# Kernel tuning notes

Measured on AMD Instinct MI355X. Metric: run time of the kernel, lower is better.

Reference implementation:

```python
import jax, jax.numpy as jnp
import numpy as np

N_INST = 2_000_000   # total instances
D_IN = 32
D_HID = 64
D_OUT = 1
NUM_BAGS = 100_000   # ids in [0, NUM_BAGS)


def setup_inputs() -> dict:
    key = jax.random.key(0)
    k0, k1, k2, k3, k4 = jax.random.split(key, 5)
    x = jax.random.normal(k0, (N_INST, D_IN), dtype=jnp.float32)
    # sorted bag ids, every bag present (contiguous bags of equal size -> a
    # valid instance of sorted_randint over [0, NUM_BAGS))
    ids = (jnp.arange(N_INST, dtype=jnp.int32) // (N_INST // NUM_BAGS))[None, :]
    W1 = jax.random.normal(k1, (D_IN, D_HID), dtype=jnp.float32) / np.sqrt(D_IN)
    b1 = jax.random.normal(k2, (D_HID,), dtype=jnp.float32) * 0.01
    W2 = jax.random.normal(k3, (D_HID, D_OUT), dtype=jnp.float32) / np.sqrt(D_HID)
    b2 = jax.random.normal(k4, (D_OUT,), dtype=jnp.float32) * 0.01
    return {"x": x, "ids": ids, "W1": W1, "b1": b1, "W2": W2, "b2": b2}


def reference(x, ids, W1, b1, W2, b2):
    inner_ids = ids[-1]                                    # [N] bag id per instance
    h = jax.nn.relu(x @ W1 + b1)                           # prepNN: [N, D_HID]
    # fused segment mean over bags (replaces the Python loop + boolean masks)
    sums = jax.ops.segment_sum(h, inner_ids, num_segments=NUM_BAGS)          # [B, D_HID]
    counts = jax.ops.segment_sum(jnp.ones((h.shape[0],), h.dtype), inner_ids,
                                 num_segments=NUM_BAGS)                      # [B]
    pooled = sums / counts[:, None]                        # aggregation_func = mean
    out = pooled @ W2 + b2                                 # afterNN: [B, D_OUT]
    return out
```

## Files before the change

kernel.cpp:

```cpp
#include <hip/hip_runtime.h>

typedef __attribute__((ext_vector_type(8))) short short8v;
typedef __attribute__((ext_vector_type(4))) int   int4v;
typedef __attribute__((ext_vector_type(4))) float f32x4;

#define NBLOCKS 1024
#define WPB 4
#define NSLOT 64

__device__ __forceinline__ unsigned short f2bf(float f) {
  unsigned u = __builtin_bit_cast(unsigned, f);
  unsigned r = u + 0x7FFFu + ((u >> 16) & 1u);
  return (unsigned short)(r >> 16);
}
__device__ __forceinline__ float bf2f(unsigned short h) {
  unsigned u = ((unsigned)h) << 16;
  return __builtin_bit_cast(float, u);
}

template <int CTRL>
__device__ __forceinline__ float dpp_add(float s) {
  int t = __builtin_amdgcn_update_dpp(0, __builtin_bit_cast(int, s), CTRL, 0xF, 0xF, true);
  return s + __builtin_bit_cast(float, t);
}

__global__ void __launch_bounds__(256) bag_mlp_v3(
    const float* __restrict__ x, const int* __restrict__ ids,
    const float* __restrict__ W1, const float* __restrict__ b1,
    const float* __restrict__ W2,
    float* __restrict__ bag_sum, int nchunks, int cpw, int nbags)
{
  __shared__ __align__(16) char stage[WPB][8192];
  __shared__ float sacc[WPB][NSLOT];

  const int wid  = threadIdx.x >> 6;
  const int lane = threadIdx.x & 63;
  const int lm = lane & 15, lg = lane >> 4;
  const int w = blockIdx.x * WPB + wid;

  const int c_begin = w * cpw;
  if (c_begin >= nchunks) return;
  const int c_end = min(c_begin + cpw, nchunks);

  sacc[wid][lane] = 0.f;
  const int base_id = ids[(size_t)c_begin * 64];

  short8v bh[4], bl[4];
#pragma unroll
  for (int nt = 0; nt < 4; ++nt) {
    const int col = lm + 16 * nt;
#pragma unroll
    for (int e = 0; e < 8; ++e) {
      const int k = 16 * (e >> 2) + 4 * lg + (e & 3);
      const float f = W1[k * 64 + col];
      const unsigned short h = f2bf(f);
      bh[nt][e] = (short)h;
      bl[nt][e] = (short)f2bf(f - bf2f(h));
    }
  }
  float b1c[4], w2c[4];
#pragma unroll
  for (int nt = 0; nt < 4; ++nt) {
    b1c[nt] = b1[lm + 16 * nt];
    w2c[nt] = W2[lm + 16 * nt];
  }

  const int R_perm = ((lm >> 2) << 4) + (lg << 2) + (lm & 3);

  auto issue_stage = [&](int c) {
    const float* src0 = x + (size_t)c * 2048;
#pragma unroll
    for (int q = 0; q < 8; ++q) {
      const int g   = q * 64 + lane;
      const int row = g >> 3;
      const int sl  = (g & 7) ^ (row & 7);
      const float* src = src0 + row * 32 + sl * 4;
      __builtin_amdgcn_global_load_lds(
          (const __attribute__((address_space(1))) void*)src,
          (__attribute__((address_space(3))) void*)(&stage[wid][q * 1024]),
          16, 0, 0);
    }
  };

  issue_stage(c_begin);

  for (int c = c_begin; c < c_end; ++c) {
    asm volatile("s_waitcnt vmcnt(0)" ::: "memory");

    const int myid = ids[(size_t)c * 64 + R_perm];

    short8v ah[4], al[4];
    const char* sb = &stage[wid][0];
#pragma unroll
    for (int t = 0; t < 4; ++t) {
      const int rb = t * 2048 + lm * 128;
      const float4 va = *(const float4*)(sb + rb + ((lg ^ (lm & 7)) << 4));
      const float4 vb = *(const float4*)(sb + rb + (((lg + 4) ^ (lm & 7)) << 4));
      int4v ahi, ali;
#pragma unroll
      for (int j = 0; j < 4; ++j) {
        const float f0 = (j < 2) ? ((j == 0) ? va.x : va.z) : ((j == 2) ? vb.x : vb.z);
        const float f1 = (j < 2) ? ((j == 0) ? va.y : va.w) : ((j == 2) ? vb.y : vb.w);
        const unsigned u0 = __builtin_bit_cast(unsigned, f0);
        const unsigned u1 = __builtin_bit_cast(unsigned, f1);
        const unsigned r0 = u0 + 0x7FFFu + ((u0 >> 16) & 1u);
        const unsigned r1 = u1 + 0x7FFFu + ((u1 >> 16) & 1u);
        const unsigned h0 = r0 & 0xFFFF0000u, h1 = r1 & 0xFFFF0000u;
        const float lo0 = f0 - __builtin_bit_cast(float, h0);
        const float lo1 = f1 - __builtin_bit_cast(float, h1);
        ahi[j] = (int)((r0 >> 16) | h1);
        ali[j] = (int)(((unsigned)f2bf(lo0)) | (((unsigned)f2bf(lo1)) << 16));
      }
      ah[t] = __builtin_bit_cast(short8v, ahi);
      al[t] = __builtin_bit_cast(short8v, ali);
    }

    asm volatile("s_waitcnt lgkmcnt(0)" ::: "memory");
    const int cnext = (c + 1 < c_end) ? c + 1 : c;
    issue_stage(cnext);

    float myval = 0.f;
#pragma unroll
    for (int t = 0; t < 4; ++t) {
      f32x4 acc[4];
#pragma unroll
      for (int nt = 0; nt < 4; ++nt)
        acc[nt] = (f32x4){b1c[nt], b1c[nt], b1c[nt], b1c[nt]};
#pragma unroll
      for (int nt = 0; nt < 4; ++nt) {
        acc[nt] = __builtin_amdgcn_mfma_f32_16x16x32_bf16(ah[t], bh[nt], acc[nt], 0, 0, 0);
        acc[nt] = __builtin_amdgcn_mfma_f32_16x16x32_bf16(ah[t], bl[nt], acc[nt], 0, 0, 0);
        acc[nt] = __builtin_amdgcn_mfma_f32_16x16x32_bf16(al[t], bh[nt], acc[nt], 0, 0, 0);
      }
      float ps[4];
#pragma unroll
      for (int r = 0; r < 4; ++r) {
        float s = 0.f;
#pragma unroll
        for (int nt = 0; nt < 4; ++nt)
          s = fmaf(fmaxf(acc[nt][r], 0.f), w2c[nt], s);
        ps[r] = s;
      }
#pragma unroll
      for (int r = 0; r < 4; ++r) {
        ps[r] = dpp_add<0xB1>(ps[r]);
        ps[r] = dpp_add<0x4E>(ps[r]);
        ps[r] = dpp_add<0x124>(ps[r]);
        ps[r] = dpp_add<0x128>(ps[r]);
      }
      const float t01 = (lm & 1) ? ps[1] : ps[0];
      const float t23 = (lm & 1) ? ps[3] : ps[2];
      const float sel = (lm & 2) ? t23 : t01;
      if ((lm >> 2) == t) myval = sel;
    }

    const int slot = myid - base_id;
    if (slot < NSLOT) atomicAdd(&sacc[wid][slot], myval);
    else              atomicAdd(&bag_sum[myid], myval);
  }

  const float v = sacc[wid][lane];
  const int bag = base_id + lane;
  if (v != 0.f && bag < nbags) atomicAdd(&bag_sum[bag], v);
}

__global__ void __launch_bounds__(256) bag_start_kernel(
    const int* __restrict__ ids, int* __restrict__ start, int n)
{
  for (int i = blockIdx.x * blockDim.x + threadIdx.x; i < n;
       i += gridDim.x * blockDim.x) {
    const int id = ids[i];
    if (i == 0 || ids[i - 1] != id) start[id] = i;
  }
}

__global__ void __launch_bounds__(256) finalize_kernel(
    const float* __restrict__ bag_sum, const int* __restrict__ start,
    const float* __restrict__ b2, float* __restrict__ out, int nbags, int n)
{
  const int b = blockIdx.x * blockDim.x + threadIdx.x;
  if (b >= nbags) return;
  const int s = start[b];
  const int e = (b + 1 < nbags) ? start[b + 1] : n;
  out[b] = bag_sum[b] / (float)(e - s) + b2[0];
}

extern "C" void kernel_launch(void* const* d_in, const int* in_sizes, int n_in,
                              void* d_out, int out_size, void* d_ws, size_t ws_size,
                              hipStream_t stream)
{
  const float* x   = (const float*)d_in[0];
  const int*   ids = (const int*)d_in[1];
  const float* W1  = (const float*)d_in[2];
  const float* b1  = (const float*)d_in[3];
  const float* W2  = (const float*)d_in[4];
  const float* b2  = (const float*)d_in[5];
  float* out = (float*)d_out;

  const int n     = in_sizes[0] / 32;
  const int nbags = out_size;

  float* bag_sum = (float*)d_ws;
  int*   start   = (int*)(bag_sum + nbags);

  (void)hipMemsetAsync(bag_sum, 0, (size_t)nbags * sizeof(float), stream);

  const int nchunks = n / 64;
  const int nwaves  = NBLOCKS * WPB;
  const int cpw     = (nchunks + nwaves - 1) / nwaves;

  bag_mlp_v3<<<NBLOCKS, 256, 0, stream>>>(x, ids, W1, b1, W2, bag_sum,
                                          nchunks, cpw, nbags);
  bag_start_kernel<<<2048, 256, 0, stream>>>(ids, start, n);
  finalize_kernel<<<(nbags + 255) / 256, 256, 0, stream>>>(bag_sum, start, b2,
                                                           out, nbags, n);
}
```

Baseline: 366.5 us.

## Prefetch next chunk into registers and use truncation for bf16 split

Replaces the direct global-to-LDS async loads with register prefetching: each iteration writes the previously loaded chunk to LDS, then issues global loads for the next chunk (and its ids) that overlap with the MFMA compute. The bf16 hi/lo split now truncates instead of rounding, which removes several integer ops per element, and launch bounds request three blocks per CU. The changes trade more register pressure and extra LDS store instructions for less exposed load latency and less conversion work. Truncation slightly changes the precision of the three-term split.

```diff
diff --git a/kernel.cpp b/kernel.cpp
--- a/kernel.cpp
+++ b/kernel.cpp
@@ -24,7 +24,7 @@
   return s + __builtin_bit_cast(float, t);
 }
 
-__global__ void __launch_bounds__(256) bag_mlp_v3(
+__global__ void __launch_bounds__(256, 3) bag_mlp_v4(
     const float* __restrict__ x, const int* __restrict__ ids,
     const float* __restrict__ W1, const float* __restrict__ b1,
     const float* __restrict__ W2,
@@ -66,58 +66,61 @@
   }
 
   const int R_perm = ((lm >> 2) << 4) + (lg << 2) + (lm & 3);
-
-  auto issue_stage = [&](int c) {
-    const float* src0 = x + (size_t)c * 2048;
-#pragma unroll
-    for (int q = 0; q < 8; ++q) {
-      const int g   = q * 64 + lane;
-      const int row = g >> 3;
-      const int sl  = (g & 7) ^ (row & 7);
-      const float* src = src0 + row * 32 + sl * 4;
-      __builtin_amdgcn_global_load_lds(
-          (const __attribute__((address_space(1))) void*)src,
-          (__attribute__((address_space(3))) void*)(&stage[wid][q * 1024]),
-          16, 0, 0);
-    }
-  };
-
-  issue_stage(c_begin);
+  const int wr_base = (lane >> 3) * 128 + ((((lane & 7) ^ ((lane >> 3) & 7))) << 4);
+  char* sb = &stage[wid][0];
+
+  float4 r0, r1, r2, r3, r4, r5, r6, r7;
+  int myid;
+  {
+    const float4* src = (const float4*)(x + (size_t)c_begin * 2048) + lane;
+    r0 = src[0];   r1 = src[64];  r2 = src[128]; r3 = src[192];
+    r4 = src[256]; r5 = src[320]; r6 = src[384]; r7 = src[448];
+    myid = ids[(size_t)c_begin * 64 + R_perm];
+  }
 
   for (int c = c_begin; c < c_end; ++c) {
-    asm volatile("s_waitcnt vmcnt(0)" ::: "memory");
-
-    const int myid = ids[(size_t)c * 64 + R_perm];
+    asm volatile("s_waitcnt lgkmcnt(0)" ::: "memory");
+    __builtin_amdgcn_sched_barrier(0);
+
+    *(float4*)(sb + wr_base)        = r0;
+    *(float4*)(sb + wr_base + 1024) = r1;
+    *(float4*)(sb + wr_base + 2048) = r2;
+    *(float4*)(sb + wr_base + 3072) = r3;
+    *(float4*)(sb + wr_base + 4096) = r4;
+    *(float4*)(sb + wr_base + 5120) = r5;
+    *(float4*)(sb + wr_base + 6144) = r6;
+    *(float4*)(sb + wr_base + 7168) = r7;
+
+    const int cnext = (c + 1 < c_end) ? c + 1 : c;
+    const float4* nsrc = (const float4*)(x + (size_t)cnext * 2048) + lane;
+    float4 n0 = nsrc[0],   n1 = nsrc[64],  n2 = nsrc[128], n3 = nsrc[192];
+    float4 n4 = nsrc[256], n5 = nsrc[320], n6 = nsrc[384], n7 = nsrc[448];
+    const int nid = ids[(size_t)cnext * 64 + R_perm];
 
     short8v ah[4], al[4];
-    const char* sb = &stage[wid][0];
 #pragma unroll
     for (int t = 0; t < 4; ++t) {
       const int rb = t * 2048 + lm * 128;
       const float4 va = *(const float4*)(sb + rb + ((lg ^ (lm & 7)) << 4));
       const float4 vb = *(const float4*)(sb + rb + (((lg + 4) ^ (lm & 7)) << 4));
       int4v ahi, ali;
-#pragma unroll
-      for (int j = 0; j < 4; ++j) {
-        const float f0 = (j < 2) ? ((j == 0) ? va.x : va.z) : ((j == 2) ? vb.x : vb.z);
-        const float f1 = (j < 2) ? ((j == 0) ? va.y : va.w) : ((j == 2) ? vb.y : vb.w);
+      const float pf[8] = {va.x, va.y, va.z, va.w, vb.x, vb.y, vb.z, vb.w};
+#pragma unroll
+      for (int p = 0; p < 4; ++p) {
+        const float f0 = pf[2 * p], f1 = pf[2 * p + 1];
         const unsigned u0 = __builtin_bit_cast(unsigned, f0);
         const unsigned u1 = __builtin_bit_cast(unsigned, f1);
-        const unsigned r0 = u0 + 0x7FFFu + ((u0 >> 16) & 1u);
-        const unsigned r1 = u1 + 0x7FFFu + ((u1 >> 16) & 1u);
-        const unsigned h0 = r0 & 0xFFFF0000u, h1 = r1 & 0xFFFF0000u;
+        const unsigned h0 = u0 & 0xFFFF0000u, h1 = u1 & 0xFFFF0000u;
+        ahi[p] = (int)((u0 >> 16) | h1);
         const float lo0 = f0 - __builtin_bit_cast(float, h0);
         const float lo1 = f1 - __builtin_bit_cast(float, h1);
-        ahi[j] = (int)((r0 >> 16) | h1);
-        ali[j] = (int)(((unsigned)f2bf(lo0)) | (((unsigned)f2bf(lo1)) << 16));
+        const unsigned lu0 = __builtin_bit_cast(unsigned, lo0);
+        const unsigned lu1 = __builtin_bit_cast(unsigned, lo1);
+        ali[p] = (int)((lu0 >> 16) | (lu1 & 0xFFFF0000u));
       }
       ah[t] = __builtin_bit_cast(short8v, ahi);
       al[t] = __builtin_bit_cast(short8v, ali);
     }
-
-    asm volatile("s_waitcnt lgkmcnt(0)" ::: "memory");
-    const int cnext = (c + 1 < c_end) ? c + 1 : c;
-    issue_stage(cnext);
 
     float myval = 0.f;
 #pragma unroll
@@ -157,6 +160,10 @@
     const int slot = myid - base_id;
     if (slot < NSLOT) atomicAdd(&sacc[wid][slot], myval);
     else              atomicAdd(&bag_sum[myid], myval);
+
+    r0 = n0; r1 = n1; r2 = n2; r3 = n3;
+    r4 = n4; r5 = n5; r6 = n6; r7 = n7;
+    myid = nid;
   }
 
   const float v = sacc[wid][lane];
@@ -209,7 +216,7 @@
   const int nwaves  = NBLOCKS * WPB;
   const int cpw     = (nchunks + nwaves - 1) / nwaves;
 
-  bag_mlp_v3<<<NBLOCKS, 256, 0, stream>>>(x, ids, W1, b1, W2, bag_sum,
+  bag_mlp_v4<<<NBLOCKS, 256, 0, stream>>>(x, ids, W1, b1, W2, bag_sum,
                                           nchunks, cpw, nbags);
   bag_start_kernel<<<2048, 256, 0, stream>>>(ids, start, n);
   finalize_kernel<<<(nbags + 255) / 256, 256, 0, stream>>>(bag_sum, start, b2,
```

Measured after the change: 369.0 us. About the same (+0.7%).
